# Kernel optimization log

Measured on AMD Instinct MI355X. Metric: run time of the kernel, lower is better.

The kernel has to match this reference:

```python
import jax, jax.numpy as jnp
import numpy as np

B = 1048576
VEC_SZ = 4
LUT_BITS = 8
K = 2 ** LUT_BITS  # 256 codewords


def setup_inputs() -> dict:
    key = jax.random.key(0)
    kx, kt = jax.random.split(key)
    X = jax.random.normal(kx, (B, VEC_SZ), dtype=jnp.float32)
    tlut = jax.random.normal(kt, (K, VEC_SZ), dtype=jnp.float32)  # codebook [K, vec_sz]
    return {"X": X, "tlut": tlut}


def reference(X, tlut):
    # torch.cdist(X, tlut) -> argmin is equivalent to argmin of squared distances:
    x_sq = jnp.sum(X * X, axis=-1, keepdims=True)            # [B, 1]
    c_sq = jnp.sum(tlut * tlut, axis=-1)                     # [K]
    cross = jnp.einsum('bd,kd->bk', X, tlut)                 # [B, K]
    dist2 = x_sq - 2.0 * cross + c_sq                        # [B, K]
    state = jnp.argmin(dist2, axis=-1).astype(jnp.int32)     # [B]
    hatX = jnp.take(tlut, state, axis=0)                     # gather reconstruction [B, vec_sz]
    return hatX, state
```

## Files before the change

### kernel.cpp

```cpp
#include <hip/hip_runtime.h>

#define K_CW 256
#define PPT 4

__global__ void vq_csq_kernel(const float* __restrict__ tlut, float* __restrict__ csq) {
    int k = threadIdx.x;
    float c0 = tlut[k * 4 + 0];
    float c1 = tlut[k * 4 + 1];
    float c2 = tlut[k * 4 + 2];
    float c3 = tlut[k * 4 + 3];
    float s = __fadd_rn(__fadd_rn(__fadd_rn(__fmul_rn(c0, c0), __fmul_rn(c1, c1)),
                                  __fmul_rn(c2, c2)),
                        __fmul_rn(c3, c3));
    csq[k] = s;
}

__global__ __launch_bounds__(256) void vq_argmin_kernel(
    const float* __restrict__ X,
    const float* __restrict__ tlut,
    const float* __restrict__ csq,
    float* __restrict__ outX,
    float* __restrict__ outS,
    int B) {
    const int tid = blockIdx.x * blockDim.x + threadIdx.x;
    const int stride = B / PPT;
    if (tid >= stride) return;

    const float4* __restrict__ X4 = reinterpret_cast<const float4*>(X);
    const float4* __restrict__ T4 = reinterpret_cast<const float4*>(tlut);

    float x0[PPT], x1[PPT], x2[PPT], x3[PPT], xsq[PPT], bestd[PPT];
    int besti[PPT];

    #pragma unroll
    for (int i = 0; i < PPT; ++i) {
        const float4 xv = X4[tid + i * stride];
        x0[i] = xv.x; x1[i] = xv.y; x2[i] = xv.z; x3[i] = xv.w;
        xsq[i] = __fadd_rn(__fadd_rn(__fadd_rn(__fmul_rn(xv.x, xv.x), __fmul_rn(xv.y, xv.y)),
                                     __fmul_rn(xv.z, xv.z)),
                           __fmul_rn(xv.w, xv.w));
        bestd[i] = __builtin_inff();
        besti[i] = 0;
    }

    #pragma unroll 4
    for (int k = 0; k < K_CW; ++k) {
        const float4 c = T4[k];
        const float cs = csq[k];
        #pragma unroll
        for (int i = 0; i < PPT; ++i) {
            float cross = __fmul_rn(x0[i], c.x);
            cross = __fmaf_rn(x1[i], c.y, cross);
            cross = __fmaf_rn(x2[i], c.z, cross);
            cross = __fmaf_rn(x3[i], c.w, cross);
            float t = __fmaf_rn(-2.0f, cross, xsq[i]);
            float d = __fadd_rn(t, cs);
            bool lt = d < bestd[i];
            besti[i] = lt ? k : besti[i];
            bestd[i] = lt ? d : bestd[i];
        }
    }

    #pragma unroll
    for (int i = 0; i < PPT; ++i) {
        const int p = tid + i * stride;
        reinterpret_cast<float4*>(outX)[p] = T4[besti[i]];
        outS[p] = (float)besti[i];
    }
}

extern "C" void kernel_launch(void* const* d_in, const int* in_sizes, int n_in,
                              void* d_out, int out_size, void* d_ws, size_t ws_size,
                              hipStream_t stream) {
    const float* X    = (const float*)d_in[0];
    const float* tlut = (const float*)d_in[1];
    const int B = in_sizes[0] / 4;

    float* outX = (float*)d_out;
    float* outS = outX + (size_t)B * 4;

    float* csq = (float*)d_ws;

    vq_csq_kernel<<<1, 256, 0, stream>>>(tlut, csq);

    const int threads = B / PPT;
    const int block = 256;
    const int grid = (threads + block - 1) / block;
    vq_argmin_kernel<<<grid, block, 0, stream>>>(X, tlut, csq, outX, outS, B);
}
```

Measured before the change: 119.8 us.

## Split codebook search across two half-blocks and merge argmin via shared memory

```diff
diff --git a/kernel.cpp b/kernel.cpp
--- a/kernel.cpp
+++ b/kernel.cpp
@@ -2,6 +2,7 @@
 
 #define K_CW 256
 #define PPT 4
+#define KHALF 128
 
 __global__ void vq_csq_kernel(const float* __restrict__ tlut, float* __restrict__ csq) {
     int k = threadIdx.x;
@@ -15,16 +16,23 @@
     csq[k] = s;
 }
 
-__global__ __launch_bounds__(256) void vq_argmin_kernel(
+__global__ __launch_bounds__(512) void vq_argmin_kernel(
     const float* __restrict__ X,
     const float* __restrict__ tlut,
     const float* __restrict__ csq,
     float* __restrict__ outX,
     float* __restrict__ outS,
     int B) {
-    const int tid = blockIdx.x * blockDim.x + threadIdx.x;
+    __shared__ float4 sd[256];
+    __shared__ int4   si[256];
+
+    const int t = threadIdx.x;
+    const int tt = t & 255;
+    const int half = t >> 8;
+    const int kbase = __builtin_amdgcn_readfirstlane(half << 7);
+
+    const int g = blockIdx.x * 256 + tt;
     const int stride = B / PPT;
-    if (tid >= stride) return;
 
     const float4* __restrict__ X4 = reinterpret_cast<const float4*>(X);
     const float4* __restrict__ T4 = reinterpret_cast<const float4*>(tlut);
@@ -34,17 +42,18 @@
 
     #pragma unroll
     for (int i = 0; i < PPT; ++i) {
-        const float4 xv = X4[tid + i * stride];
+        const float4 xv = X4[g + i * stride];
         x0[i] = xv.x; x1[i] = xv.y; x2[i] = xv.z; x3[i] = xv.w;
         xsq[i] = __fadd_rn(__fadd_rn(__fadd_rn(__fmul_rn(xv.x, xv.x), __fmul_rn(xv.y, xv.y)),
                                      __fmul_rn(xv.z, xv.z)),
                            __fmul_rn(xv.w, xv.w));
         bestd[i] = __builtin_inff();
-        besti[i] = 0;
+        besti[i] = kbase;
     }
 
-    #pragma unroll 4
-    for (int k = 0; k < K_CW; ++k) {
+    #pragma unroll 8
+    for (int kk = 0; kk < KHALF; ++kk) {
+        const int k = kbase + kk;
         const float4 c = T4[k];
         const float cs = csq[k];
         #pragma unroll
@@ -53,19 +62,32 @@
             cross = __fmaf_rn(x1[i], c.y, cross);
             cross = __fmaf_rn(x2[i], c.z, cross);
             cross = __fmaf_rn(x3[i], c.w, cross);
-            float t = __fmaf_rn(-2.0f, cross, xsq[i]);
-            float d = __fadd_rn(t, cs);
-            bool lt = d < bestd[i];
-            besti[i] = lt ? k : besti[i];
-            bestd[i] = lt ? d : bestd[i];
+            float t2 = __fmaf_rn(-2.0f, cross, xsq[i]);
+            float d = __fadd_rn(t2, cs);
+            besti[i] = (d < bestd[i]) ? k : besti[i];
+            bestd[i] = fminf(d, bestd[i]);
         }
     }
 
-    #pragma unroll
-    for (int i = 0; i < PPT; ++i) {
-        const int p = tid + i * stride;
-        reinterpret_cast<float4*>(outX)[p] = T4[besti[i]];
-        outS[p] = (float)besti[i];
+    if (half == 1) {
+        sd[tt] = make_float4(bestd[0], bestd[1], bestd[2], bestd[3]);
+        si[tt] = make_int4(besti[0], besti[1], besti[2], besti[3]);
+    }
+    __syncthreads();
+    if (half == 0) {
+        const float4 od = sd[tt];
+        const int4   oi = si[tt];
+        if (od.x < bestd[0]) { bestd[0] = od.x; besti[0] = oi.x; }
+        if (od.y < bestd[1]) { bestd[1] = od.y; besti[1] = oi.y; }
+        if (od.z < bestd[2]) { bestd[2] = od.z; besti[2] = oi.z; }
+        if (od.w < bestd[3]) { bestd[3] = od.w; besti[3] = oi.w; }
+
+        #pragma unroll
+        for (int i = 0; i < PPT; ++i) {
+            const int p = g + i * stride;
+            reinterpret_cast<float4*>(outX)[p] = T4[besti[i]];
+            outS[p] = (float)besti[i];
+        }
     }
 }
 
@@ -83,8 +105,7 @@
 
     vq_csq_kernel<<<1, 256, 0, stream>>>(tlut, csq);
 
-    const int threads = B / PPT;
-    const int block = 256;
-    const int grid = (threads + block - 1) / block;
-    vq_argmin_kernel<<<grid, block, 0, stream>>>(X, tlut, csq, outX, outS, B);
+    const int groups = B / PPT;
+    const int grid = groups / 256;
+    vq_argmin_kernel<<<grid, 512, 0, stream>>>(X, tlut, csq, outX, outS, B);
 }
```

Result: faster. 116.2 us (-3.0%).
